# Performance work log

Measured on AMD Instinct MI355X. Metric: run time of the kernel, lower is better.

The kernel has to match this reference:

```python
import jax, jax.numpy as jnp
import numpy as np

NH, KD, VD, C = 8, 64, 64, 256

def conv1x1(x, w, b):
    # x: (B,C,D,H,W), w: (O,C), b: (O,)
    return jnp.einsum('bcdhw,oc->bodhw', x, w) + b[None, :, None, None, None]

def setup_inputs() -> dict:
    key = jax.random.key(0)
    ks = jax.random.split(key, 8)
    B, D, H, W = 2, 32, 32, 32
    s = 0.02
    return {
        'x': jax.random.normal(ks[0], (B, C, D, H, W), jnp.float32),
        'q_w': jax.random.normal(ks[1], (NH * KD, C), jnp.float32) * s,
        'q_b': jnp.zeros((NH * KD,), jnp.float32),
        'kv_w': jax.random.normal(ks[2], (KD + VD, C), jnp.float32) * s,
        'kv_b': jnp.zeros((KD + VD,), jnp.float32),
        'proj_w': jax.random.normal(ks[3], (C, NH * VD), jnp.float32) * s,
        'proj_b': jnp.zeros((C,), jnp.float32),
        'layer_scale': jnp.full((C, 1, 1, 1), 1e-5, jnp.float32),
    }

def reference(x, q_w, q_b, kv_w, kv_b, proj_w, proj_b, layer_scale):
    B, Cc, D, H, W = x.shape
    scale = VD ** -0.5
    # q: (B, nh, D, H, W, kd) -> flatten(3,5) -> (B, nh, D, H*W*kd)
    q = conv1x1(x, q_w, q_b).reshape(B, NH, KD, D, H, W).transpose(0, 1, 3, 4, 5, 2)
    q = q.reshape(B, NH, D, H * W * KD)
    kv = conv1x1(x, kv_w, kv_b)  # (B, kd+vd, D, H, W)
    k = kv[:, :KD].transpose(0, 2, 3, 4, 1).reshape(B, D, H * W * KD)  # shared across heads
    v = kv[:, KD:].transpose(0, 2, 3, 4, 1).reshape(B, D, H * W * VD)
    attn = jax.nn.softmax(jnp.einsum('bnqf,bkf->bnqk', q, k) * scale, axis=-1)  # (B,nh,D,D)
    o = jnp.einsum('bnqk,bkf->bnqf', attn, v)  # (B, nh, D, H*W*vd)
    # transpose(1,2) then row-major reshape, exactly as torch
    o = o.transpose(0, 2, 1, 3).reshape(B, D, H, W, NH * VD).transpose(0, 4, 1, 2, 3)
    out = conv1x1(o, proj_w, proj_b)
    return out * layer_scale[None]
```

## Files before the change

kernel.cpp:

```cpp
#include <hip/hip_runtime.h>
#include <math.h>

#define SS 32768

typedef _Float16 half4v __attribute__((ext_vector_type(4)));
typedef _Float16 half8v __attribute__((ext_vector_type(8)));
typedef float float4v __attribute__((ext_vector_type(4)));

__device__ __forceinline__ void gload16(const void* g, void* l) {
    __builtin_amdgcn_global_load_lds(
        (const __attribute__((address_space(1))) unsigned int*)g,
        (__attribute__((address_space(3))) unsigned int*)l, 16, 0, 0);
}

__global__ __launch_bounds__(256)
void cvt_x_kernel(const float* __restrict__ x, _Float16* __restrict__ x_t)
{
    __shared__ float ls[64][65];
    const int b = blockIdx.z, c0 = blockIdx.y * 64, s0 = blockIdx.x * 64;
    const int t = threadIdx.x;
    const int tr = t >> 4, tc = t & 15;
#pragma unroll
    for (int p = 0; p < 4; p++) {
        int c_l = p * 16 + tr;
        float4v v = *(const float4v*)(x + (size_t)(b * 256 + c0 + c_l) * SS + s0 + tc * 4);
        ls[c_l][tc * 4 + 0] = v.x;
        ls[c_l][tc * 4 + 1] = v.y;
        ls[c_l][tc * 4 + 2] = v.z;
        ls[c_l][tc * 4 + 3] = v.w;
    }
    __syncthreads();
#pragma unroll
    for (int p = 0; p < 4; p++) {
        int s_l = p * 16 + tr;
        half4v h;
        h.x = (_Float16)ls[tc * 4 + 0][s_l];
        h.y = (_Float16)ls[tc * 4 + 1][s_l];
        h.z = (_Float16)ls[tc * 4 + 2][s_l];
        h.w = (_Float16)ls[tc * 4 + 3][s_l];
        *(half4v*)(x_t + ((size_t)b * SS + s0 + s_l) * 256 + c0 + tc * 4) = h;
    }
}

__global__ __launch_bounds__(256)
void cvt_w3_kernel(const float* __restrict__ s0, _Float16* __restrict__ d0,
                   const float* __restrict__ s1, _Float16* __restrict__ d1,
                   const float* __restrict__ s2, _Float16* __restrict__ d2)
{
    int bx = blockIdx.x;
    const float* s; _Float16* d; int base;
    if (bx < 128)      { s = s0; d = d0; base = bx; }
    else if (bx < 160) { s = s1; d = d1; base = bx - 128; }
    else               { s = s2; d = d2; base = bx - 160; }
    int i = (base * 256 + threadIdx.x) * 4;
    float4v v = *(const float4v*)(s + i);
    half4v h;
    h.x = (_Float16)v.x; h.y = (_Float16)v.y; h.z = (_Float16)v.z; h.w = (_Float16)v.w;
    *(half4v*)(d + i) = h;
}

__global__ __launch_bounds__(256)
void conv_mfma_kernel(const _Float16* __restrict__ x_t,
                      const _Float16* __restrict__ wq,
                      const _Float16* __restrict__ wkv,
                      const float* __restrict__ q_b,
                      const float* __restrict__ kv_b,
                      _Float16* __restrict__ q_t,
                      _Float16* __restrict__ kv_t)
{
    __shared__ _Float16 smem[128 * 136];
    _Float16* const Ws = smem;
    _Float16* const Xs = smem + 128 * 64;
    const int b = blockIdx.y;
    const int bx = blockIdx.x;
    const int grp = bx / 40, rem = bx % 40;
    const int s_tile = grp * 8 + (rem & 7);
    const int o_tile = rem >> 3;
    const int s0 = s_tile * 128;
    const bool is_q = (o_tile < 4);
    const _Float16* W = is_q ? wq : wkv;
    const float* bias = is_q ? q_b : kv_b;
    const int od0 = is_q ? o_tile * 128 : 0;
    const int ODST = is_q ? 512 : 128;
    _Float16* dst = is_q ? q_t : kv_t;

    const int t = threadIdx.x;
    const int w = t >> 6, l = t & 63;
    const int om = (w & 1) * 64, sn = (w >> 1) * 64;

    const int lr = l >> 3;
    const int gch = ((l & 7) - lr) & 7;
    const int m15 = l & 15;
    const int sl0 = ((((l >> 4) + (l & 7)) & 7)) * 8;
    const int sl1 = ((((l >> 4) + 4 + (l & 7)) & 7)) * 8;

    float4v acc[4][4];
#pragma unroll
    for (int i = 0; i < 4; i++)
#pragma unroll
        for (int j = 0; j < 4; j++) acc[i][j] = (float4v){0.f, 0.f, 0.f, 0.f};

    const _Float16* wg = W + (size_t)(od0 + 32 * w + lr) * 256 + gch * 8;
    const _Float16* xg = x_t + ((size_t)b * SS + s0 + 32 * w + lr) * 256 + gch * 8;
    _Float16* wl = &Ws[(32 * w) * 64];
    _Float16* xl = &Xs[(32 * w) * 64];

    for (int c0 = 0; c0 < 256; c0 += 64) {
#pragma unroll
        for (int rb = 0; rb < 4; rb++) {
            gload16(wg + (size_t)rb * 8 * 256 + c0, wl + rb * 8 * 64);
            gload16(xg + (size_t)rb * 8 * 256 + c0, xl + rb * 8 * 64);
        }
        __syncthreads();
#pragma unroll
        for (int ks = 0; ks < 2; ks++) {
            const int sl = ks ? sl1 : sl0;
            half8v a[4], bb[4];
#pragma unroll
            for (int i = 0; i < 4; i++)
                a[i] = *(const half8v*)&Ws[(om + i * 16 + m15) * 64 + sl];
#pragma unroll
            for (int j = 0; j < 4; j++)
                bb[j] = *(const half8v*)&Xs[(sn + j * 16 + m15) * 64 + sl];
#pragma unroll
            for (int i = 0; i < 4; i++)
#pragma unroll
                for (int j = 0; j < 4; j++)
                    acc[i][j] = __builtin_amdgcn_mfma_f32_16x16x32_f16(a[i], bb[j], acc[i][j], 0, 0, 0);
        }
        __syncthreads();
    }
    const int qd = l >> 4, m = l & 15;
#pragma unroll
    for (int i = 0; i < 4; i++) {
        float bv[4];
#pragma unroll
        for (int r = 0; r < 4; r++) bv[r] = bias[od0 + om + i * 16 + qd * 4 + r];
#pragma unroll
        for (int j = 0; j < 4; j++) {
            half4v h;
            h.x = (_Float16)(acc[i][j].x + bv[0]);
            h.y = (_Float16)(acc[i][j].y + bv[1]);
            h.z = (_Float16)(acc[i][j].z + bv[2]);
            h.w = (_Float16)(acc[i][j].w + bv[3]);
            int s_l = sn + j * 16 + m;
            *(half4v*)&smem[s_l * 136 + om + i * 16 + qd * 4] = h;
        }
    }
    __syncthreads();
    const int sr = t >> 4, kk = t & 15;
#pragma unroll
    for (int p = 0; p < 8; p++) {
        int s_l = p * 16 + sr;
        half8v h8 = *(const half8v*)&smem[s_l * 136 + kk * 8];
        *(half8v*)(dst + ((size_t)b * SS + s0 + s_l) * ODST + od0 + kk * 8) = h8;
    }
}

__global__ __launch_bounds__(256)
void logits_kernel(const _Float16* __restrict__ q_t,
                   const _Float16* __restrict__ kv_t,
                   float* __restrict__ Lpart)
{
    __shared__ float red[4][1024];
    const int hwc = blockIdx.x, nh = blockIdx.y, b = blockIdx.z;
    const int t = threadIdx.x, w = t >> 6, l = t & 63;
    const int m = l & 15, c8 = (l >> 4) * 8;
    float4v acc[2][2];
#pragma unroll
    for (int i = 0; i < 2; i++)
#pragma unroll
        for (int j = 0; j < 2; j++) acc[i][j] = (float4v){0.f, 0.f, 0.f, 0.f};

    const _Float16* qb0 = q_t + (size_t)b * SS * 512 + nh * 64 + c8;
    const _Float16* kb0 = kv_t + (size_t)b * SS * 128 + c8;
#pragma unroll 4
    for (int hh = 0; hh < 8; hh++) {
        const int hw = hwc * 32 + w * 8 + hh;
        const _Float16* qr0 = qb0 + ((size_t)m * 1024 + hw) * 512;
        const _Float16* qr1 = qb0 + ((size_t)(m + 16) * 1024 + hw) * 512;
        const _Float16* kr0 = kb0 + ((size_t)m * 1024 + hw) * 128;
        const _Float16* kr1 = kb0 + ((size_t)(m + 16) * 1024 + hw) * 128;
        half8v a0l = *(const half8v*)(qr0);
        half8v a0h = *(const half8v*)(qr0 + 32);
        half8v a1l = *(const half8v*)(qr1);
        half8v a1h = *(const half8v*)(qr1 + 32);
        half8v b0l = *(const half8v*)(kr0);
        half8v b0h = *(const half8v*)(kr0 + 32);
        half8v b1l = *(const half8v*)(kr1);
        half8v b1h = *(const half8v*)(kr1 + 32);
        acc[0][0] = __builtin_amdgcn_mfma_f32_16x16x32_f16(a0l, b0l, acc[0][0], 0, 0, 0);
        acc[0][0] = __builtin_amdgcn_mfma_f32_16x16x32_f16(a0h, b0h, acc[0][0], 0, 0, 0);
        acc[0][1] = __builtin_amdgcn_mfma_f32_16x16x32_f16(a0l, b1l, acc[0][1], 0, 0, 0);
        acc[0][1] = __builtin_amdgcn_mfma_f32_16x16x32_f16(a0h, b1h, acc[0][1], 0, 0, 0);
        acc[1][0] = __builtin_amdgcn_mfma_f32_16x16x32_f16(a1l, b0l, acc[1][0], 0, 0, 0);
        acc[1][0] = __builtin_amdgcn_mfma_f32_16x16x32_f16(a1h, b0h, acc[1][0], 0, 0, 0);
        acc[1][1] = __builtin_amdgcn_mfma_f32_16x16x32_f16(a1l, b1l, acc[1][1], 0, 0, 0);
        acc[1][1] = __builtin_amdgcn_mfma_f32_16x16x32_f16(a1h, b1h, acc[1][1], 0, 0, 0);
    }
    const int rbase = (l >> 4) * 4;
#pragma unroll
    for (int qi = 0; qi < 2; qi++)
#pragma unroll
        for (int qj = 0; qj < 2; qj++)
#pragma unroll
            for (int rr = 0; rr < 4; rr++)
                red[w][(qi * 16 + rbase + rr) * 32 + qj * 16 + m] = acc[qi][qj][rr];
    __syncthreads();
    float4v v = *(const float4v*)&red[0][t * 4];
    v += *(const float4v*)&red[1][t * 4];
    v += *(const float4v*)&red[2][t * 4];
    v += *(const float4v*)&red[3][t * 4];
    *(float4v*)(Lpart + (((size_t)hwc * 2 + b) * 8 + nh) * 1024 + t * 4) = v;
}

__global__ __launch_bounds__(256)
void softmax_kernel(const float* __restrict__ Lpart, float* __restrict__ Lsm)
{
    int r = blockIdx.x * 256 + threadIdx.x;
    float4v p[8];
#pragma unroll
    for (int j4 = 0; j4 < 8; j4++) p[j4] = (float4v){0.f, 0.f, 0.f, 0.f};
    for (int hwc = 0; hwc < 32; hwc++) {
        const float* src = Lpart + (size_t)hwc * 16384 + (size_t)r * 32;
#pragma unroll
        for (int j4 = 0; j4 < 8; j4++) p[j4] += *(const float4v*)(src + j4 * 4);
    }
    float mx = p[0].x;
#pragma unroll
    for (int j4 = 0; j4 < 8; j4++) {
        mx = fmaxf(mx, p[j4].x); mx = fmaxf(mx, p[j4].y);
        mx = fmaxf(mx, p[j4].z); mx = fmaxf(mx, p[j4].w);
    }
    float s = 0.f;
#pragma unroll
    for (int j4 = 0; j4 < 8; j4++) {
        p[j4].x = expf((p[j4].x - mx) * 0.125f); s += p[j4].x;
        p[j4].y = expf((p[j4].y - mx) * 0.125f); s += p[j4].y;
        p[j4].z = expf((p[j4].z - mx) * 0.125f); s += p[j4].z;
        p[j4].w = expf((p[j4].w - mx) * 0.125f); s += p[j4].w;
    }
    float inv = 1.f / s;
    float* dst = Lsm + (size_t)r * 32;
#pragma unroll
    for (int j4 = 0; j4 < 8; j4++) {
        float4v o = p[j4];
        o.x *= inv; o.y *= inv; o.z *= inv; o.w *= inv;
        *(float4v*)(dst + j4 * 4) = o;
    }
}

__global__ __launch_bounds__(256)
void attn_v_kernel(const _Float16* __restrict__ kv_t,
                   const float* __restrict__ attn,
                   _Float16* __restrict__ o_t)
{
    __shared__ float as_[2048];
    const int wq = blockIdx.x, hl = blockIdx.y;
    const int b = blockIdx.z >> 2, rc = blockIdx.z & 3;
    const int t = threadIdx.x;
    {
        const float* src = attn + (size_t)b * 8192 + rc * 2048;
#pragma unroll
        for (int ll = 0; ll < 2; ll++) {
            int idx = (t + ll * 256) * 4;
            *(float4v*)(&as_[idx]) = *(const float4v*)(src + idx);
        }
    }
    __syncthreads();
    const int q4 = t & 127;
    const int half = t >> 7;
    const int tt = q4 >> 4;
    const int vd = (q4 * 4) & 63;
    const int hw = hl * 256 + wq * 8 + tt;
    float4v vreg[32];
#pragma unroll
    for (int j = 0; j < 32; j++) {
        half4v hv = *(const half4v*)(kv_t + ((size_t)((b * 32 + j) * 1024 + hw)) * 128 + 64 + vd);
        vreg[j] = (float4v){(float)hv.x, (float)hv.y, (float)hv.z, (float)hv.w};
    }
    _Float16* outb = o_t + (size_t)b * SS * 512;
#pragma unroll 2
    for (int rr = 0; rr < 32; rr++) {
        int row_l = half * 32 + rr;
        int row = rc * 64 + row_l;
        int hh = row >> 5, d = row & 31;
        const float* arow = &as_[row_l * 32];
        float ax = 0.f, ay = 0.f, az = 0.f, aw = 0.f;
#pragma unroll
        for (int j4 = 0; j4 < 8; j4++) {
            float4v a4 = *(const float4v*)(&arow[j4 * 4]);
            float4v v0 = vreg[j4 * 4 + 0];
            float4v v1 = vreg[j4 * 4 + 1];
            float4v v2 = vreg[j4 * 4 + 2];
            float4v v3 = vreg[j4 * 4 + 3];
            ax = fmaf(a4.x, v0.x, ax); ay = fmaf(a4.x, v0.y, ay);
            az = fmaf(a4.x, v0.z, az); aw = fmaf(a4.x, v0.w, aw);
            ax = fmaf(a4.y, v1.x, ax); ay = fmaf(a4.y, v1.y, ay);
            az = fmaf(a4.y, v1.z, az); aw = fmaf(a4.y, v1.w, aw);
            ax = fmaf(a4.z, v2.x, ax); ay = fmaf(a4.z, v2.y, ay);
            az = fmaf(a4.z, v2.z, az); aw = fmaf(a4.z, v2.w, aw);
            ax = fmaf(a4.w, v3.x, ax); ay = fmaf(a4.w, v3.y, ay);
            az = fmaf(a4.w, v3.z, az); aw = fmaf(a4.w, v3.w, aw);
        }
        int hp = hh * 4 + hl;
        size_t sp = (size_t)d * 1024 + hp * 32 + wq;
        half4v o4;
        o4.x = (_Float16)ax; o4.y = (_Float16)ay; o4.z = (_Float16)az; o4.w = (_Float16)aw;
        *(half4v*)(outb + sp * 512 + q4 * 4) = o4;
    }
}

__global__ __launch_bounds__(256)
void proj_mfma_kernel(const _Float16* __restrict__ o_t,
                      const _Float16* __restrict__ wp,
                      const float* __restrict__ pb,
                      const float* __restrict__ ls,
                      float* __restrict__ out)
{
    __shared__ _Float16 Ws[128 * 64];
    __shared__ _Float16 Xs[128 * 64];
    const int b = blockIdx.y;
    const int bx = blockIdx.x;
    const int grp = bx >> 4, rem = bx & 15;
    const int s_tile = grp * 8 + (rem & 7);
    const int o_tile = rem >> 3;
    const int s0 = s_tile * 128, o0 = o_tile * 128;
    const int t = threadIdx.x;
    const int w = t >> 6, l = t & 63;
    const int om = (w & 1) * 64, sn = (w >> 1) * 64;

    const int lr = l >> 3;
    const int gch = ((l & 7) - lr) & 7;
    const int m15 = l & 15;
    const int sl0 = ((((l >> 4) + (l & 7)) & 7)) * 8;
    const int sl1 = ((((l >> 4) + 4 + (l & 7)) & 7)) * 8;

    float4v acc[4][4];
#pragma unroll
    for (int i = 0; i < 4; i++)
#pragma unroll
        for (int j = 0; j < 4; j++) acc[i][j] = (float4v){0.f, 0.f, 0.f, 0.f};

    const _Float16* wg = wp + (size_t)(o0 + 32 * w + lr) * 512 + gch * 8;
    const _Float16* xg = o_t + ((size_t)b * SS + s0 + 32 * w + lr) * 512 + gch * 8;
    _Float16* wl = &Ws[(32 * w) * 64];
    _Float16* xl = &Xs[(32 * w) * 64];

    for (int c0 = 0; c0 < 512; c0 += 64) {
#pragma unroll
        for (int rb = 0; rb < 4; rb++) {
            gload16(wg + (size_t)rb * 8 * 512 + c0, wl + rb * 8 * 64);
            gload16(xg + (size_t)rb * 8 * 512 + c0, xl + rb * 8 * 64);
        }
        __syncthreads();
#pragma unroll
        for (int ks = 0; ks < 2; ks++) {
            const int sl = ks ? sl1 : sl0;
            half8v a[4], bb[4];
#pragma unroll
            for (int i = 0; i < 4; i++)
                a[i] = *(const half8v*)&Ws[(om + i * 16 + m15) * 64 + sl];
#pragma unroll
            for (int j = 0; j < 4; j++)
                bb[j] = *(const half8v*)&Xs[(sn + j * 16 + m15) * 64 + sl];
#pragma unroll
            for (int i = 0; i < 4; i++)
#pragma unroll
                for (int j = 0; j < 4; j++)
                    acc[i][j] = __builtin_amdgcn_mfma_f32_16x16x32_f16(a[i], bb[j], acc[i][j], 0, 0, 0);
        }
        __syncthreads();
    }
    const int qd = l >> 4, m = l & 15;
#pragma unroll
    for (int i = 0; i < 4; i++) {
        float pbv[4], lsv[4];
#pragma unroll
        for (int r = 0; r < 4; r++) {
            int o = o0 + om + i * 16 + qd * 4 + r;
            pbv[r] = pb[o];
            lsv[r] = ls[o];
        }
#pragma unroll
        for (int j = 0; j < 4; j++) {
            int s = s0 + sn + j * 16 + m;
#pragma unroll
            for (int r = 0; r < 4; r++) {
                int o = o0 + om + i * 16 + qd * 4 + r;
                out[((size_t)b * 256 + o) * SS + s] = (acc[i][j][r] + pbv[r]) * lsv[r];
            }
        }
    }
}

extern "C" void kernel_launch(void* const* d_in, const int* in_sizes, int n_in,
                              void* d_out, int out_size, void* d_ws, size_t ws_size,
                              hipStream_t stream)
{
    const float* x      = (const float*)d_in[0];
    const float* q_w    = (const float*)d_in[1];
    const float* q_b    = (const float*)d_in[2];
    const float* kv_w   = (const float*)d_in[3];
    const float* kv_b   = (const float*)d_in[4];
    const float* proj_w = (const float*)d_in[5];
    const float* proj_b = (const float*)d_in[6];
    const float* ls     = (const float*)d_in[7];
    float* out = (float*)d_out;

    char* ws = (char*)d_ws;
    _Float16* x_t  = (_Float16*)(ws);
    _Float16* q_t  = (_Float16*)(ws + 33554432);
    _Float16* kv_t = (_Float16*)(ws + 100663296);
    float*    Lpart= (float*)   (ws + 117440512);
    float*    Lsm  = (float*)   (ws + 119537664);
    _Float16* wq   = (_Float16*)(ws + 119603200);
    _Float16* wkv  = (_Float16*)(ws + 119865344);
    _Float16* wp   = (_Float16*)(ws + 119930880);
    _Float16* o_t  = q_t;

    cvt_x_kernel<<<dim3(512, 4, 2), 256, 0, stream>>>(x, x_t);
    cvt_w3_kernel<<<dim3(288), 256, 0, stream>>>(q_w, wq, kv_w, wkv, proj_w, wp);

    conv_mfma_kernel<<<dim3(1280, 2), 256, 0, stream>>>(x_t, wq, wkv, q_b, kv_b, q_t, kv_t);
    logits_kernel<<<dim3(32, 8, 2), 256, 0, stream>>>(q_t, kv_t, Lpart);
    softmax_kernel<<<dim3(2), 256, 0, stream>>>(Lpart, Lsm);
    attn_v_kernel<<<dim3(32, 4, 8), 256, 0, stream>>>(kv_t, Lsm, o_t);
    proj_mfma_kernel<<<dim3(512, 2), 256, 0, stream>>>(o_t, wp, proj_b, ls, out);
}
```

Baseline: 283.6 us.

## Fuse Q projection into logits kernel to avoid materializing Q tensor

Measured after the change: 259.2 us. -8.6%, faster.

```diff
diff --git a/kernel.cpp b/kernel.cpp
--- a/kernel.cpp
+++ b/kernel.cpp
@@ -2,6 +2,7 @@
 #include <math.h>
 
 #define SS 32768
+#define FQL_LDS_BYTES 147456
 
 typedef _Float16 half4v __attribute__((ext_vector_type(4)));
 typedef _Float16 half8v __attribute__((ext_vector_type(8)));
@@ -60,30 +61,16 @@
 }
 
 __global__ __launch_bounds__(256)
-void conv_mfma_kernel(const _Float16* __restrict__ x_t,
-                      const _Float16* __restrict__ wq,
-                      const _Float16* __restrict__ wkv,
-                      const float* __restrict__ q_b,
-                      const float* __restrict__ kv_b,
-                      _Float16* __restrict__ q_t,
-                      _Float16* __restrict__ kv_t)
+void convkv_kernel(const _Float16* __restrict__ x_t,
+                   const _Float16* __restrict__ wkv,
+                   const float* __restrict__ kv_b,
+                   _Float16* __restrict__ kv_t)
 {
     __shared__ _Float16 smem[128 * 136];
     _Float16* const Ws = smem;
     _Float16* const Xs = smem + 128 * 64;
     const int b = blockIdx.y;
-    const int bx = blockIdx.x;
-    const int grp = bx / 40, rem = bx % 40;
-    const int s_tile = grp * 8 + (rem & 7);
-    const int o_tile = rem >> 3;
-    const int s0 = s_tile * 128;
-    const bool is_q = (o_tile < 4);
-    const _Float16* W = is_q ? wq : wkv;
-    const float* bias = is_q ? q_b : kv_b;
-    const int od0 = is_q ? o_tile * 128 : 0;
-    const int ODST = is_q ? 512 : 128;
-    _Float16* dst = is_q ? q_t : kv_t;
-
+    const int s0 = blockIdx.x * 128;
     const int t = threadIdx.x;
     const int w = t >> 6, l = t & 63;
     const int om = (w & 1) * 64, sn = (w >> 1) * 64;
@@ -100,7 +87,7 @@
 #pragma unroll
         for (int j = 0; j < 4; j++) acc[i][j] = (float4v){0.f, 0.f, 0.f, 0.f};
 
-    const _Float16* wg = W + (size_t)(od0 + 32 * w + lr) * 256 + gch * 8;
+    const _Float16* wg = wkv + (size_t)(32 * w + lr) * 256 + gch * 8;
     const _Float16* xg = x_t + ((size_t)b * SS + s0 + 32 * w + lr) * 256 + gch * 8;
     _Float16* wl = &Ws[(32 * w) * 64];
     _Float16* xl = &Xs[(32 * w) * 64];
@@ -135,7 +122,7 @@
     for (int i = 0; i < 4; i++) {
         float bv[4];
 #pragma unroll
-        for (int r = 0; r < 4; r++) bv[r] = bias[od0 + om + i * 16 + qd * 4 + r];
+        for (int r = 0; r < 4; r++) bv[r] = kv_b[om + i * 16 + qd * 4 + r];
 #pragma unroll
         for (int j = 0; j < 4; j++) {
             half4v h;
@@ -153,101 +140,162 @@
     for (int p = 0; p < 8; p++) {
         int s_l = p * 16 + sr;
         half8v h8 = *(const half8v*)&smem[s_l * 136 + kk * 8];
-        *(half8v*)(dst + ((size_t)b * SS + s0 + s_l) * ODST + od0 + kk * 8) = h8;
-    }
-}
-
-__global__ __launch_bounds__(256)
-void logits_kernel(const _Float16* __restrict__ q_t,
-                   const _Float16* __restrict__ kv_t,
-                   float* __restrict__ Lpart)
-{
-    __shared__ float red[4][1024];
-    const int hwc = blockIdx.x, nh = blockIdx.y, b = blockIdx.z;
-    const int t = threadIdx.x, w = t >> 6, l = t & 63;
-    const int m = l & 15, c8 = (l >> 4) * 8;
-    float4v acc[2][2];
-#pragma unroll
-    for (int i = 0; i < 2; i++)
-#pragma unroll
-        for (int j = 0; j < 2; j++) acc[i][j] = (float4v){0.f, 0.f, 0.f, 0.f};
-
-    const _Float16* qb0 = q_t + (size_t)b * SS * 512 + nh * 64 + c8;
-    const _Float16* kb0 = kv_t + (size_t)b * SS * 128 + c8;
-#pragma unroll 4
-    for (int hh = 0; hh < 8; hh++) {
-        const int hw = hwc * 32 + w * 8 + hh;
-        const _Float16* qr0 = qb0 + ((size_t)m * 1024 + hw) * 512;
-        const _Float16* qr1 = qb0 + ((size_t)(m + 16) * 1024 + hw) * 512;
-        const _Float16* kr0 = kb0 + ((size_t)m * 1024 + hw) * 128;
-        const _Float16* kr1 = kb0 + ((size_t)(m + 16) * 1024 + hw) * 128;
-        half8v a0l = *(const half8v*)(qr0);
-        half8v a0h = *(const half8v*)(qr0 + 32);
-        half8v a1l = *(const half8v*)(qr1);
-        half8v a1h = *(const half8v*)(qr1 + 32);
-        half8v b0l = *(const half8v*)(kr0);
-        half8v b0h = *(const half8v*)(kr0 + 32);
-        half8v b1l = *(const half8v*)(kr1);
-        half8v b1h = *(const half8v*)(kr1 + 32);
-        acc[0][0] = __builtin_amdgcn_mfma_f32_16x16x32_f16(a0l, b0l, acc[0][0], 0, 0, 0);
-        acc[0][0] = __builtin_amdgcn_mfma_f32_16x16x32_f16(a0h, b0h, acc[0][0], 0, 0, 0);
-        acc[0][1] = __builtin_amdgcn_mfma_f32_16x16x32_f16(a0l, b1l, acc[0][1], 0, 0, 0);
-        acc[0][1] = __builtin_amdgcn_mfma_f32_16x16x32_f16(a0h, b1h, acc[0][1], 0, 0, 0);
-        acc[1][0] = __builtin_amdgcn_mfma_f32_16x16x32_f16(a1l, b0l, acc[1][0], 0, 0, 0);
-        acc[1][0] = __builtin_amdgcn_mfma_f32_16x16x32_f16(a1h, b0h, acc[1][0], 0, 0, 0);
-        acc[1][1] = __builtin_amdgcn_mfma_f32_16x16x32_f16(a1l, b1l, acc[1][1], 0, 0, 0);
-        acc[1][1] = __builtin_amdgcn_mfma_f32_16x16x32_f16(a1h, b1h, acc[1][1], 0, 0, 0);
-    }
-    const int rbase = (l >> 4) * 4;
-#pragma unroll
-    for (int qi = 0; qi < 2; qi++)
-#pragma unroll
-        for (int qj = 0; qj < 2; qj++)
+        *(half8v*)(kv_t + ((size_t)b * SS + s0 + s_l) * 128 + kk * 8) = h8;
+    }
+}
+
+__global__ __launch_bounds__(512)
+void fq_logits_kernel(const _Float16* __restrict__ x_t,
+                      const _Float16* __restrict__ wq,
+                      const float* __restrict__ q_b,
+                      const _Float16* __restrict__ kv_t,
+                      float* __restrict__ Lpart)
+{
+    extern __shared__ _Float16 sm[];
+    _Float16* const Xs = sm;
+    _Float16* const W0 = sm + 32768;
+    _Float16* const W1 = sm + 49152;
+    _Float16* const Qs = sm + 65536;
+
+    const int chunk = blockIdx.x, b = blockIdx.y;
+    const int hw0 = chunk * 4;
+    const int t = threadIdx.x;
+    const int w = t >> 6, l = t & 63;
+    const int lq = l >> 4;
+    const int l15 = l & 15;
+    const int rh = l >> 5, ch = l & 31;
+
+#pragma unroll
+    for (int i = 0; i < 8; i++) {
+        int r = w * 16 + i * 2 + rh;
+        int qd = r >> 2, hwl = r & 3;
+        int sc = ch ^ (r & 7);
+        gload16(x_t + ((size_t)b * SS + qd * 1024 + hw0 + hwl) * 256 + sc * 8,
+                Xs + (w * 16 + i * 2) * 256);
+    }
+#pragma unroll
+    for (int i = 0; i < 4; i++) {
+        int r = w * 8 + i * 2 + rh;
+        int sc = ch ^ (r & 7);
+        gload16(wq + (size_t)r * 256 + sc * 8, W0 + (w * 8 + i * 2) * 256);
+    }
+
+    half8v bk[8];
+    if (w < 4) {
+        const int nj = w & 1;
+        const int kd = nj * 16 + l15;
+        const _Float16* kbase = kv_t + ((size_t)b * SS + (size_t)kd * 1024 + hw0) * 128;
+#pragma unroll
+        for (int ks = 0; ks < 8; ks++) {
+            int kk = ks * 32 + lq * 8;
+            bk[ks] = *(const half8v*)(kbase + (size_t)(kk >> 6) * 128 + (kk & 63));
+        }
+    }
+    __syncthreads();
+
+    const int wm = w >> 2, wn = w & 3;
+    const int m0 = wm * 32, n0 = wn * 32;
+    float* const lp_base = Lpart + (((size_t)chunk * 2 + b) * 8) * 1024;
+
+    for (int nh = 0; nh < 8; nh++) {
+        _Float16* const Wcur = (nh & 1) ? W1 : W0;
+        if (nh < 7) {
+            _Float16* const Wnxt = (nh & 1) ? W0 : W1;
+#pragma unroll
+            for (int i = 0; i < 4; i++) {
+                int r = w * 8 + i * 2 + rh;
+                int sc = ch ^ (r & 7);
+                gload16(wq + ((size_t)((nh + 1) * 64 + r)) * 256 + sc * 8,
+                        Wnxt + (w * 8 + i * 2) * 256);
+            }
+        }
+        float4v qacc[2][2];
+#pragma unroll
+        for (int i = 0; i < 2; i++)
+#pragma unroll
+            for (int j = 0; j < 2; j++) qacc[i][j] = (float4v){0.f, 0.f, 0.f, 0.f};
+#pragma unroll
+        for (int ks = 0; ks < 8; ks++) {
+            int c8 = (ks * 32 + lq * 8) ^ ((l & 7) << 3);
+            half8v a0 = *(const half8v*)&Wcur[(m0 + l15) * 256 + c8];
+            half8v a1 = *(const half8v*)&Wcur[(m0 + 16 + l15) * 256 + c8];
+            half8v x0 = *(const half8v*)&Xs[(n0 + l15) * 256 + c8];
+            half8v x1 = *(const half8v*)&Xs[(n0 + 16 + l15) * 256 + c8];
+            qacc[0][0] = __builtin_amdgcn_mfma_f32_16x16x32_f16(a0, x0, qacc[0][0], 0, 0, 0);
+            qacc[0][1] = __builtin_amdgcn_mfma_f32_16x16x32_f16(a0, x1, qacc[0][1], 0, 0, 0);
+            qacc[1][0] = __builtin_amdgcn_mfma_f32_16x16x32_f16(a1, x0, qacc[1][0], 0, 0, 0);
+            qacc[1][1] = __builtin_amdgcn_mfma_f32_16x16x32_f16(a1, x1, qacc[1][1], 0, 0, 0);
+        }
+        __syncthreads();
+#pragma unroll
+        for (int i = 0; i < 2; i++) {
+            int kbase = m0 + i * 16 + lq * 4;
+            float4v bv = *(const float4v*)(q_b + nh * 64 + kbase);
+#pragma unroll
+            for (int j = 0; j < 2; j++) {
+                int sp = n0 + j * 16 + l15;
+                int key = ((sp ^ (sp >> 2)) & 7) << 3;
+                half4v h;
+                h.x = (_Float16)(qacc[i][j].x + bv.x);
+                h.y = (_Float16)(qacc[i][j].y + bv.y);
+                h.z = (_Float16)(qacc[i][j].z + bv.z);
+                h.w = (_Float16)(qacc[i][j].w + bv.w);
+                *(half4v*)&Qs[sp * 64 + (kbase ^ key)] = h;
+            }
+        }
+        __syncthreads();
+        if (w < 4) {
+            const int mi = w >> 1, nj = w & 1;
+            const int qd = mi * 16 + l15;
+            float4v lacc = (float4v){0.f, 0.f, 0.f, 0.f};
+#pragma unroll
+            for (int ks = 0; ks < 8; ks++) {
+                int kk = ks * 32 + lq * 8;
+                int sp = qd * 4 + (kk >> 6);
+                int key = ((sp ^ (sp >> 2)) & 7) << 3;
+                half8v a = *(const half8v*)&Qs[sp * 64 + ((kk & 63) ^ key)];
+                lacc = __builtin_amdgcn_mfma_f32_16x16x32_f16(a, bk[ks], lacc, 0, 0, 0);
+            }
+            float* dst = lp_base + (size_t)nh * 1024;
 #pragma unroll
             for (int rr = 0; rr < 4; rr++)
-                red[w][(qi * 16 + rbase + rr) * 32 + qj * 16 + m] = acc[qi][qj][rr];
+                dst[(mi * 16 + lq * 4 + rr) * 32 + nj * 16 + l15] = lacc[rr];
+        }
+    }
+}
+
+__global__ __launch_bounds__(256)
+void softmax_kernel(const float* __restrict__ Lpart, float* __restrict__ Lsm)
+{
+    __shared__ float red[32][8][32];
+    const int t = threadIdx.x;
+    const int rl = t & 7, cs = t >> 3;
+    const int row = blockIdx.x * 8 + rl;
+    const int b = row >> 8, nh = (row >> 5) & 7, qd = row & 31;
+    float4v p[8];
+#pragma unroll
+    for (int j4 = 0; j4 < 8; j4++) p[j4] = (float4v){0.f, 0.f, 0.f, 0.f};
+    for (int cc = 0; cc < 8; cc++) {
+        int chunk = cs + cc * 32;
+        const float* src = Lpart + (((size_t)chunk * 2 + b) * 8 + nh) * 1024 + qd * 32;
+#pragma unroll
+        for (int j4 = 0; j4 < 8; j4++) p[j4] += *(const float4v*)(src + j4 * 4);
+    }
+#pragma unroll
+    for (int j4 = 0; j4 < 8; j4++) *(float4v*)&red[cs][rl][j4 * 4] = p[j4];
     __syncthreads();
-    float4v v = *(const float4v*)&red[0][t * 4];
-    v += *(const float4v*)&red[1][t * 4];
-    v += *(const float4v*)&red[2][t * 4];
-    v += *(const float4v*)&red[3][t * 4];
-    *(float4v*)(Lpart + (((size_t)hwc * 2 + b) * 8 + nh) * 1024 + t * 4) = v;
-}
-
-__global__ __launch_bounds__(256)
-void softmax_kernel(const float* __restrict__ Lpart, float* __restrict__ Lsm)
-{
-    int r = blockIdx.x * 256 + threadIdx.x;
-    float4v p[8];
-#pragma unroll
-    for (int j4 = 0; j4 < 8; j4++) p[j4] = (float4v){0.f, 0.f, 0.f, 0.f};
-    for (int hwc = 0; hwc < 32; hwc++) {
-        const float* src = Lpart + (size_t)hwc * 16384 + (size_t)r * 32;
-#pragma unroll
-        for (int j4 = 0; j4 < 8; j4++) p[j4] += *(const float4v*)(src + j4 * 4);
-    }
-    float mx = p[0].x;
-#pragma unroll
-    for (int j4 = 0; j4 < 8; j4++) {
-        mx = fmaxf(mx, p[j4].x); mx = fmaxf(mx, p[j4].y);
-        mx = fmaxf(mx, p[j4].z); mx = fmaxf(mx, p[j4].w);
-    }
+    const int r2 = t >> 5, j = t & 31;
     float s = 0.f;
 #pragma unroll
-    for (int j4 = 0; j4 < 8; j4++) {
-        p[j4].x = expf((p[j4].x - mx) * 0.125f); s += p[j4].x;
-        p[j4].y = expf((p[j4].y - mx) * 0.125f); s += p[j4].y;
-        p[j4].z = expf((p[j4].z - mx) * 0.125f); s += p[j4].z;
-        p[j4].w = expf((p[j4].w - mx) * 0.125f); s += p[j4].w;
-    }
-    float inv = 1.f / s;
-    float* dst = Lsm + (size_t)r * 32;
-#pragma unroll
-    for (int j4 = 0; j4 < 8; j4++) {
-        float4v o = p[j4];
-        o.x *= inv; o.y *= inv; o.z *= inv; o.w *= inv;
-        *(float4v*)(dst + j4 * 4) = o;
-    }
+    for (int c2 = 0; c2 < 32; c2++) s += red[c2][r2][j];
+    float mx = s;
+#pragma unroll
+    for (int off = 16; off >= 1; off >>= 1) mx = fmaxf(mx, __shfl_xor(mx, off, 32));
+    float e = expf((s - mx) * 0.125f);
+    float sum = e;
+#pragma unroll
+    for (int off = 16; off >= 1; off >>= 1) sum += __shfl_xor(sum, off, 32);
+    Lsm[(size_t)(blockIdx.x * 8 + r2) * 32 + j] = e / sum;
 }
 
 __global__ __launch_bounds__(256)
@@ -410,21 +458,27 @@
 
     char* ws = (char*)d_ws;
     _Float16* x_t  = (_Float16*)(ws);
-    _Float16* q_t  = (_Float16*)(ws + 33554432);
+    _Float16* o_t  = (_Float16*)(ws + 33554432);
+    float*    Lpart= (float*)   (ws + 33554432);
     _Float16* kv_t = (_Float16*)(ws + 100663296);
-    float*    Lpart= (float*)   (ws + 117440512);
-    float*    Lsm  = (float*)   (ws + 119537664);
-    _Float16* wq   = (_Float16*)(ws + 119603200);
-    _Float16* wkv  = (_Float16*)(ws + 119865344);
-    _Float16* wp   = (_Float16*)(ws + 119930880);
-    _Float16* o_t  = q_t;
+    float*    Lsm  = (float*)   (ws + 117440512);
+    _Float16* wq   = (_Float16*)(ws + 117506048);
+    _Float16* wkv  = (_Float16*)(ws + 117768192);
+    _Float16* wp   = (_Float16*)(ws + 117833728);
+
+    static bool fql_attr_set = false;
+    if (!fql_attr_set) {
+        hipFuncSetAttribute(reinterpret_cast<const void*>(fq_logits_kernel),
+                            hipFuncAttributeMaxDynamicSharedMemorySize, FQL_LDS_BYTES);
+        fql_attr_set = true;
+    }
 
     cvt_x_kernel<<<dim3(512, 4, 2), 256, 0, stream>>>(x, x_t);
     cvt_w3_kernel<<<dim3(288), 256, 0, stream>>>(q_w, wq, kv_w, wkv, proj_w, wp);
 
-    conv_mfma_kernel<<<dim3(1280, 2), 256, 0, stream>>>(x_t, wq, wkv, q_b, kv_b, q_t, kv_t);
-    logits_kernel<<<dim3(32, 8, 2), 256, 0, stream>>>(q_t, kv_t, Lpart);
-    softmax_kernel<<<dim3(2), 256, 0, stream>>>(Lpart, Lsm);
+    convkv_kernel<<<dim3(256, 2), 256, 0, stream>>>(x_t, wkv, kv_b, kv_t);
+    fq_logits_kernel<<<dim3(256, 2), 512, FQL_LDS_BYTES, stream>>>(x_t, wq, q_b, kv_t, Lpart);
+    softmax_kernel<<<dim3(64), 256, 0, stream>>>(Lpart, Lsm);
     attn_v_kernel<<<dim3(32, 4, 8), 256, 0, stream>>>(kv_t, Lsm, o_t);
     proj_mfma_kernel<<<dim3(512, 2), 256, 0, stream>>>(o_t, wp, proj_b, ls, out);
 }
```
